# Kernel tuning notes

Measured on AMD Instinct MI355X. Metric: run time of the kernel, lower is better.

The kernel has to match this reference:

```python
import jax, jax.numpy as jnp
import numpy as np

DIM = 512
HEADS = 8
HD = DIM // HEADS
HIDDEN = 4 * DIM
EPS = 1e-5


def layernorm(x, g, b):
    mu = jnp.mean(x, axis=-1, keepdims=True)
    var = jnp.mean(jnp.square(x - mu), axis=-1, keepdims=True)
    return (x - mu) * jax.lax.rsqrt(var + EPS) * g + b


def setup_inputs() -> dict:
    key = jax.random.key(0)
    ks = jax.random.split(key, 10)
    B, P, N, C = 16, 4, 256, DIM
    s = 1.0 / np.sqrt(C)
    sh = 1.0 / np.sqrt(HIDDEN)
    return {
        "x": jax.random.normal(ks[0], (B, P, N, C), jnp.float32),
        "ln1_g": jnp.ones((C,), jnp.float32),
        "ln1_b": jnp.zeros((C,), jnp.float32),
        "w_qkv": jax.random.uniform(ks[1], (3 * C, C), jnp.float32, -s, s),
        "w_proj": jax.random.uniform(ks[2], (C, C), jnp.float32, -s, s),
        "b_proj": jax.random.uniform(ks[3], (C,), jnp.float32, -s, s),
        "ln2_g": jnp.ones((C,), jnp.float32),
        "ln2_b": jnp.zeros((C,), jnp.float32),
        "w1": jax.random.uniform(ks[4], (HIDDEN, C), jnp.float32, -s, s),
        "b1": jax.random.uniform(ks[5], (HIDDEN,), jnp.float32, -s, s),
        "w2": jax.random.uniform(ks[6], (C, HIDDEN), jnp.float32, -sh, sh),
        "b2": jax.random.uniform(ks[7], (C,), jnp.float32, -sh, sh),
    }


def reference(x, ln1_g, ln1_b, w_qkv, w_proj, b_proj, ln2_g, ln2_b, w1, b1, w2, b2):
    B, P, N, C = x.shape
    # --- attention branch (batched over B, P, heads; same math as the unrolled loops) ---
    h = layernorm(x, ln1_g, ln1_b)
    qkv = jnp.einsum('bpnc,dc->bpnd', h, w_qkv)            # [B,P,N,3C]
    qkv = qkv.reshape(B, P, N, 3, HEADS, HD)
    q, k, v = qkv[..., 0, :, :], qkv[..., 1, :, :], qkv[..., 2, :, :]  # [B,P,N,H,hd]
    scale = HD ** -0.5
    attn = jnp.einsum('bpnhd,bpmhd->bphnm', q * scale, k)  # [B,P,H,N,N]
    attn = jax.nn.softmax(attn, axis=-1)
    o = jnp.einsum('bphnm,bpmhd->bpnhd', attn, v).reshape(B, P, N, C)
    o = jnp.einsum('bpnc,dc->bpnd', o, w_proj) + b_proj
    x = x + o
    # --- MLP branch ---
    h = layernorm(x, ln2_g, ln2_b)
    h = jax.nn.gelu(jnp.einsum('bpnc,hc->bpnh', h, w1) + b1, approximate=False)
    h = jnp.einsum('bpnh,ch->bpnc', h, w2) + b2
    return x + h
```

## Files before the change

### kernel.cpp

```cpp
#include <hip/hip_runtime.h>

typedef __attribute__((ext_vector_type(8))) short short8;
typedef __attribute__((ext_vector_type(4))) float f32x4;
typedef __attribute__((ext_vector_type(4))) unsigned short u16x4;
typedef __attribute__((ext_vector_type(2))) unsigned int u32x2;

__device__ __forceinline__ float bf2f(unsigned short u) {
    return __uint_as_float(((unsigned)u) << 16);
}
__device__ __forceinline__ unsigned short f2bf(float f) {
    unsigned u = __float_as_uint(f);
    u += 0x7fffu + ((u >> 16) & 1u);
    return (unsigned short)(u >> 16);
}
__device__ __forceinline__ unsigned pack2(float lo, float hi) {
    return (unsigned)f2bf(lo) | ((unsigned)f2bf(hi) << 16);
}
__device__ __forceinline__ void load_lds16(const void* g, void* l) {
    __builtin_amdgcn_global_load_lds(
        (const __attribute__((address_space(1))) void*)g,
        (__attribute__((address_space(3))) void*)l, 16, 0, 0);
}
__device__ __forceinline__ bool is_bf16(const unsigned* dt) {
    return *dt == 0x3F803F80u;
}
__device__ __forceinline__ float gelu_fast(float t) {
    float q = t * (1.5957691f + 0.07135482f * t * t);
    float e = __expf(-q);
    return __fdividef(t, 1.0f + e);
}

__global__ __launch_bounds__(512) void cast_all(
    const void* s_wqkv, const void* s_wproj, const void* s_w1, const void* s_w2,
    const void* v0, const void* v1, const void* v2, const void* v3,
    const void* v4, const void* v5, const void* v6,
    unsigned short* d_wqkv, unsigned short* d_wproj, unsigned short* d_w1,
    unsigned short* d_w2, unsigned short* par, const unsigned* dt)
{
    bool isbf = is_bf16(dt);
    int b = blockIdx.x, tid = threadIdx.x;
    if (b < 768) {
        const void* src; unsigned short* dst; int off;
        if (b < 192)      { src = s_wqkv;  dst = d_wqkv;  off = b * 4096; }
        else if (b < 256) { src = s_wproj; dst = d_wproj; off = (b - 192) * 4096; }
        else if (b < 512) { src = s_w1;    dst = d_w1;    off = (b - 256) * 4096; }
        else              { src = s_w2;    dst = d_w2;    off = (b - 512) * 4096; }
        int i = off + tid * 8;
        if (isbf) {
            *(short8*)(dst + i) = *(const short8*)((const unsigned short*)src + i);
        } else {
            const float* s = (const float*)src + i;
            short8 o;
            #pragma unroll
            for (int j = 0; j < 8; ++j) o[j] = (short)f2bf(s[j]);
            *(short8*)(dst + i) = o;
        }
    } else {
        const void* srcs[7]  = {v0, v1, v2, v3, v4, v5, v6};
        const int   sizes[7] = {512, 512, 512, 512, 512, 2048, 512};
        const int   offs[7]  = {0, 512, 1024, 1536, 2048, 2560, 4608};
        int j = b - 768;
        const void* s = srcs[j];
        unsigned short* d = par + offs[j];
        for (int i = tid; i < sizes[j]; i += 512)
            d[i] = isbf ? ((const unsigned short*)s)[i] : f2bf(((const float*)s)[i]);
    }
}

__global__ __launch_bounds__(256) void ln_kernel(
    const void* __restrict__ xin, size_t row0,
    const unsigned* __restrict__ dt, int inmode,
    const unsigned short* __restrict__ g, const unsigned short* __restrict__ b,
    unsigned short* __restrict__ y)
{
    int w = threadIdx.x >> 6, lane = threadIdx.x & 63;
    size_t lr = (size_t)blockIdx.x * 4 + w;
    size_t gr = row0 + lr;
    bool isf32 = (inmode == 1) || (inmode == 0 && !is_bf16(dt));
    float v[8];
    if (isf32) {
        const float* xr = (const float*)xin + (gr << 9) + (lane << 3);
        #pragma unroll
        for (int j = 0; j < 8; ++j) v[j] = xr[j];
    } else {
        short8 raw = *(const short8*)((const unsigned short*)xin + (gr << 9) + (lane << 3));
        #pragma unroll
        for (int j = 0; j < 8; ++j) v[j] = bf2f((unsigned short)raw[j]);
    }
    float sum = 0.f, sq = 0.f;
    #pragma unroll
    for (int j = 0; j < 8; ++j) { sum += v[j]; sq += v[j] * v[j]; }
    #pragma unroll
    for (int off = 32; off > 0; off >>= 1) {
        sum += __shfl_xor(sum, off);
        sq  += __shfl_xor(sq, off);
    }
    float mu  = sum * (1.0f / 512.0f);
    float var = sq * (1.0f / 512.0f) - mu * mu;
    float rs  = rsqrtf(var + 1e-5f);
    short8 gr8 = *(const short8*)(g + (lane << 3));
    short8 br8 = *(const short8*)(b + (lane << 3));
    short8 outv;
    #pragma unroll
    for (int j = 0; j < 8; ++j) {
        float o = (v[j] - mu) * rs * bf2f((unsigned short)gr8[j]) + bf2f((unsigned short)br8[j]);
        outv[j] = (short)f2bf(o);
    }
    *(short8*)(y + (lr << 9) + (lane << 3)) = outv;
}

__global__ __launch_bounds__(256, 2) void gemm8(
    const unsigned short* __restrict__ A, const unsigned short* __restrict__ W,
    const unsigned short* __restrict__ bias,
    const void* __restrict__ resid, size_t rrow0,
    void* __restrict__ out, size_t orow0,
    int NBY, int N, int K, int mode, const unsigned* __restrict__ dt)
{
    constexpr int BN = 128;
    constexpr int BUFB = 32768;
    __shared__ char lds[2 * BUFB];

    int tid = threadIdx.x;
    int w = tid >> 6, lane = tid & 63;
    int l15 = lane & 15, g = lane >> 4;

    int L = blockIdx.x;
    int bx, by;
    if ((NBY & 7) == 0) {
        int nby8 = NBY >> 3;
        int xcd = L & 7, i = L >> 3;
        by = xcd * nby8 + (i % nby8);
        bx = i / nby8;
    } else {
        by = L % NBY;
        bx = L / NBY;
    }
    int m0 = by << 7, n0 = bx << 7;
    int wm = (w >> 1) << 6;
    int wn = (w & 1) << 6;

    int srow_t = tid >> 3;
    int u_t = (tid & 7) ^ (srow_t & 7);
    const unsigned short* gA[4];
    const unsigned short* gB[4];
    #pragma unroll
    for (int j = 0; j < 4; ++j) {
        gA[j] = A + (size_t)(m0 + j * 32 + srow_t) * K + u_t * 8;
        gB[j] = W + (size_t)(n0 + j * 32 + srow_t) * K + u_t * 8;
    }
    int lslot = tid * 16;
    int swz = l15 & 7;

    f32x4 acc[4][4];
    #pragma unroll
    for (int i = 0; i < 4; ++i)
        #pragma unroll
        for (int j = 0; j < 4; ++j) acc[i][j] = (f32x4){0.f, 0.f, 0.f, 0.f};

    #pragma unroll
    for (int j = 0; j < 4; ++j) {
        load_lds16(gA[j], &lds[j * 4096 + lslot]);
        load_lds16(gB[j], &lds[16384 + j * 4096 + lslot]);
    }

    int p = 0;
    for (int k = 0; k < K; k += 64) {
        __syncthreads();
        if (k + 64 < K) {
            int kn = k + 64;
            char* nb = &lds[(p ^ 1) * BUFB];
            #pragma unroll
            for (int j = 0; j < 4; ++j) {
                load_lds16(gA[j] + kn, nb + j * 4096 + lslot);
                load_lds16(gB[j] + kn, nb + 16384 + j * 4096 + lslot);
            }
        }
        const char* bAct = &lds[p * BUFB];
        const char* bW = bAct + 16384;
        #pragma unroll
        for (int s = 0; s < 2; ++s) {
            int cs = ((s * 4 + g) ^ swz) << 4;
            short8 wf[4], af[4];
            #pragma unroll
            for (int i = 0; i < 4; ++i)
                wf[i] = *(const short8*)(bW + (wn + i * 16 + l15) * 128 + cs);
            #pragma unroll
            for (int j = 0; j < 4; ++j)
                af[j] = *(const short8*)(bAct + (wm + j * 16 + l15) * 128 + cs);
            #pragma unroll
            for (int i = 0; i < 4; ++i)
                #pragma unroll
                for (int j = 0; j < 4; ++j)
                    acc[i][j] = __builtin_amdgcn_mfma_f32_16x16x32_bf16(wf[i], af[j], acc[i][j], 0, 0, 0);
        }
        p ^= 1;
    }

    if (mode == 2) {
        #pragma unroll
        for (int i = 0; i < 4; ++i) {
            u16x4 bb = *(const u16x4*)(bias + n0 + wn + i * 16 + g * 4);
            #pragma unroll
            for (int j = 0; j < 4; ++j)
                #pragma unroll
                for (int r = 0; r < 4; ++r)
                    acc[i][j][r] = gelu_fast(acc[i][j][r] + bf2f(bb[r]));
        }
    }

    char* tb = (char*)lds;
    #pragma unroll
    for (int j = 0; j < 4; ++j) {
        int mloc = wm + j * 16 + l15;
        char* rowp = tb + mloc * (BN * 2);
        int sw = mloc & (BN / 4 - 2);
        #pragma unroll
        for (int i = 0; i < 4; ++i) {
            int cq = (wn + i * 16 + g * 4) >> 2;
            u32x2 pk = {pack2(acc[i][j][0], acc[i][j][1]),
                        pack2(acc[i][j][2], acc[i][j][3])};
            *(u32x2*)(rowp + ((cq ^ sw) << 3)) = pk;
        }
    }
    __syncthreads();

    int rL = tid >> 4;
    int lc = tid & 15;
    bool inbf = is_bf16(dt);
    int colg = n0 + lc * 8;
    float bv[8];
    if (mode == 1 || mode == 3) {
        short8 bb = *(const short8*)(bias + colg);
        #pragma unroll
        for (int t = 0; t < 8; ++t) bv[t] = bf2f((unsigned short)bb[t]);
    }

    #pragma unroll
    for (int ps = 0; ps < 8; ++ps) {
        int row = ps * 16 + rL;
        int rowL = m0 + row;
        int c16 = lc ^ ((row >> 1) & 15);
        short8 vv = *(const short8*)(tb + row * (BN * 2) + (c16 << 4));

        if (mode == 0 || mode == 2) {
            *(short8*)((unsigned short*)out + (size_t)rowL * N + colg) = vv;
        } else if (mode == 1) {
            size_t rbase = (rrow0 + rowL) * (size_t)N + colg;
            float o8[8];
            if (inbf) {
                short8 rr = *(const short8*)((const unsigned short*)resid + rbase);
                #pragma unroll
                for (int t = 0; t < 8; ++t)
                    o8[t] = bf2f((unsigned short)rr[t]) + bf2f((unsigned short)vv[t]) + bv[t];
            } else {
                f32x4 r0 = *(const f32x4*)((const float*)resid + rbase);
                f32x4 r1 = *(const f32x4*)((const float*)resid + rbase + 4);
                #pragma unroll
                for (int t = 0; t < 4; ++t) {
                    o8[t]     = r0[t] + bf2f((unsigned short)vv[t]) + bv[t];
                    o8[t + 4] = r1[t] + bf2f((unsigned short)vv[t + 4]) + bv[t + 4];
                }
            }
            short8 ov;
            #pragma unroll
            for (int t = 0; t < 8; ++t) ov[t] = (short)f2bf(o8[t]);
            *(short8*)((unsigned short*)out + (size_t)rowL * N + colg) = ov;
        } else {
            size_t rbase = (size_t)rowL * N + colg;
            short8 rr = *(const short8*)((const unsigned short*)resid + rbase);
            float o8[8];
            #pragma unroll
            for (int t = 0; t < 8; ++t)
                o8[t] = bf2f((unsigned short)rr[t]) + bf2f((unsigned short)vv[t]) + bv[t];
            size_t obase = (orow0 + rowL) * (size_t)N + colg;
            if (inbf) {
                short8 ov;
                #pragma unroll
                for (int t = 0; t < 8; ++t) ov[t] = (short)f2bf(o8[t]);
                *(short8*)((unsigned short*)out + obase) = ov;
            } else {
                float* ob = (float*)out + obase;
                *(f32x4*)ob       = (f32x4){o8[0], o8[1], o8[2], o8[3]};
                *(f32x4*)(ob + 4) = (f32x4){o8[4], o8[5], o8[6], o8[7]};
            }
        }
    }
}

__global__ __launch_bounds__(256) void attn_mfma(
    const unsigned short* __restrict__ qkv, unsigned short* __restrict__ o)
{
    __shared__ unsigned short Vt[64 * 256];
    __shared__ unsigned short Ps[4][16 * 256];
    int bp = blockIdx.x >> 3, h = blockIdx.x & 7;
    const unsigned short* base = qkv + (size_t)bp * 256 * 1536;
    int qo = h << 6, ko = 512 + (h << 6), vo = 1024 + (h << 6);
    int tid = threadIdx.x, w = tid >> 6, lane = tid & 63;
    int l15 = lane & 15, g = lane >> 4;

    {
        int d = tid & 63;
        for (int s = tid >> 6; s < 256; s += 4) {
            unsigned short v = base[(size_t)s * 1536 + vo + d];
            *(unsigned short*)((char*)Vt + d * 512 + (((s >> 3) ^ (d & 7)) << 4) + ((s & 7) << 1)) = v;
        }
    }
    __syncthreads();

    unsigned short* P = Ps[w];

    for (int pass = 0; pass < 4; ++pass) {
        int q0 = pass * 64 + w * 16;
        short8 qa[2];
        #pragma unroll
        for (int t = 0; t < 2; ++t)
            qa[t] = *(const short8*)(base + (size_t)(q0 + l15) * 1536 + qo + t * 32 + g * 8);
        f32x4 S[16];
        #pragma unroll
        for (int ns = 0; ns < 16; ++ns) {
            f32x4 a = {0.f, 0.f, 0.f, 0.f};
            #pragma unroll
            for (int t = 0; t < 2; ++t) {
                short8 kb = *(const short8*)(base + (size_t)(ns * 16 + l15) * 1536 + ko + t * 32 + g * 8);
                a = __builtin_amdgcn_mfma_f32_16x16x32_bf16(qa[t], kb, a, 0, 0, 0);
            }
            S[ns] = a;
        }
        float mx[4], sums[4], inv[4];
        #pragma unroll
        for (int r = 0; r < 4; ++r) {
            float m = -1e30f;
            #pragma unroll
            for (int ns = 0; ns < 16; ++ns) m = fmaxf(m, S[ns][r]);
            m *= 0.125f;
            #pragma unroll
            for (int off = 1; off < 16; off <<= 1) m = fmaxf(m, __shfl_xor(m, off));
            mx[r] = m;
            sums[r] = 0.f;
        }
        #pragma unroll
        for (int ns = 0; ns < 16; ++ns)
            #pragma unroll
            for (int r = 0; r < 4; ++r) {
                float p = __expf(S[ns][r] * 0.125f - mx[r]);
                sums[r] += p;
                S[ns][r] = p;
            }
        #pragma unroll
        for (int r = 0; r < 4; ++r) {
            float s2 = sums[r];
            #pragma unroll
            for (int off = 1; off < 16; off <<= 1) s2 += __shfl_xor(s2, off);
            inv[r] = 1.0f / s2;
        }
        #pragma unroll
        for (int ns = 0; ns < 16; ++ns)
            #pragma unroll
            for (int r = 0; r < 4; ++r) {
                int mq = g * 4 + r;
                int s = ns * 16 + l15;
                *(unsigned short*)((char*)P + mq * 512 + (((s >> 3) ^ (mq & 7)) << 4) + ((s & 7) << 1))
                    = f2bf(S[ns][r] * inv[r]);
            }
        f32x4 O[4];
        #pragma unroll
        for (int ds = 0; ds < 4; ++ds) O[ds] = (f32x4){0.f, 0.f, 0.f, 0.f};
        #pragma unroll
        for (int ks = 0; ks < 8; ++ks) {
            int c = (ks * 4 + g) ^ (l15 & 7);
            short8 pa = *(const short8*)((const char*)P + l15 * 512 + (c << 4));
            #pragma unroll
            for (int ds = 0; ds < 4; ++ds) {
                short8 vb = *(const short8*)((const char*)Vt + (ds * 16 + l15) * 512 + (c << 4));
                O[ds] = __builtin_amdgcn_mfma_f32_16x16x32_bf16(pa, vb, O[ds], 0, 0, 0);
            }
        }
        #pragma unroll
        for (int ds = 0; ds < 4; ++ds)
            #pragma unroll
            for (int r = 0; r < 4; ++r) {
                int mq = q0 + g * 4 + r;
                int d = ds * 16 + l15;
                o[((size_t)(bp * 256 + mq) << 9) + (h << 6) + d] = f2bf(O[ds][r]);
            }
    }
}

extern "C" void kernel_launch(void* const* d_in, const int* in_sizes, int n_in,
                              void* d_out, int out_size, void* d_ws, size_t ws_size,
                              hipStream_t stream)
{
    const void* x      = d_in[0];
    const void* ln1_g  = d_in[1];
    const void* ln1_b  = d_in[2];
    const void* w_qkv  = d_in[3];
    const void* w_proj = d_in[4];
    const void* b_proj = d_in[5];
    const void* ln2_g  = d_in[6];
    const void* ln2_b  = d_in[7];
    const void* w1     = d_in[8];
    const void* b1     = d_in[9];
    const void* w2     = d_in[10];
    const void* b2     = d_in[11];
    const unsigned* dt = (const unsigned*)ln1_g;

    const int M = 16384;
    char* ws = (char*)d_ws;
    unsigned short* wqkv_b  = (unsigned short*)(ws);
    unsigned short* wproj_b = (unsigned short*)(ws + 1572864);
    unsigned short* w1_b    = (unsigned short*)(ws + 2097152);
    unsigned short* w2_b    = (unsigned short*)(ws + 4194304);
    unsigned short* par     = (unsigned short*)(ws + 6291456);
    const size_t CAST_END = 6308096;

    unsigned short* p_g1    = par + 0;
    unsigned short* p_b1ln  = par + 512;
    unsigned short* p_bproj = par + 1024;
    unsigned short* p_g2    = par + 1536;
    unsigned short* p_b2ln  = par + 2048;
    unsigned short* p_b1    = par + 2560;
    unsigned short* p_b2    = par + 4608;

    int NC = 64;
    const int cand[7] = {1, 2, 4, 8, 16, 32, 64};
    for (int i = 0; i < 7; ++i) {
        size_t need = CAST_END + (size_t)(M / cand[i]) * 10240;
        if (need <= ws_size) { NC = cand[i]; break; }
    }
    const int R = M / NC;

    char* cb = ws + CAST_END;
    unsigned short* h   = (unsigned short*)(cb);
    unsigned short* qkv = (unsigned short*)(cb + (size_t)R * 1024);
    unsigned short* o   = (unsigned short*)(cb + (size_t)R * 4096);
    unsigned short* x2  = (unsigned short*)(cb + (size_t)R * 5120);
    unsigned short* hid = (unsigned short*)(cb + (size_t)R * 6144);
    unsigned short* h2  = h;

    cast_all<<<775, 512, 0, stream>>>(w_qkv, w_proj, w1, w2,
                                      ln1_g, ln1_b, b_proj, ln2_g, ln2_b, b1, b2,
                                      wqkv_b, wproj_b, w1_b, w2_b, par, dt);

    for (int c = 0; c < NC; ++c) {
        const size_t r0 = (size_t)c * R;
        const int NBY = R / 128;

        ln_kernel<<<R / 4, 256, 0, stream>>>(x, r0, dt, 0, p_g1, p_b1ln, h);
        gemm8<<<(1536 / 128) * NBY, 256, 0, stream>>>(
            h, wqkv_b, nullptr, nullptr, 0, qkv, 0, NBY, 1536, 512, 0, dt);
        attn_mfma<<<(R / 256) * 8, 256, 0, stream>>>(qkv, o);
        gemm8<<<(512 / 128) * NBY, 256, 0, stream>>>(
            o, wproj_b, p_bproj, x, r0, x2, 0, NBY, 512, 512, 1, dt);
        ln_kernel<<<R / 4, 256, 0, stream>>>(x2, 0, dt, 2, p_g2, p_b2ln, h2);
        gemm8<<<(2048 / 128) * NBY, 256, 0, stream>>>(
            h2, w1_b, p_b1, nullptr, 0, hid, 0, NBY, 2048, 512, 2, dt);
        gemm8<<<(512 / 128) * NBY, 256, 0, stream>>>(
            hid, w2_b, p_b2, x2, 0, d_out, r0, NBY, 512, 2048, 3, dt);
    }
}
```

Before: 320.7 us.

## Use 256x128 GEMM tiles with 512 threads and triple-buffered LDS pipeline

Doubles the GEMM M tile to 256 rows and runs 8 waves per block. The K loop moves from a double-buffered to a three-stage LDS pipeline, with prefetch two steps ahead and global loads split around the MFMA phases. It also raises wave priority around the MFMA clusters and uses explicit waitcnt/barrier scheduling. The aim is more reuse of the weight tile and better overlap of loads with compute, at the cost of 144KB of LDS per block, lower occupancy and half as many blocks.

```diff
diff --git a/kernel.cpp b/kernel.cpp
--- a/kernel.cpp
+++ b/kernel.cpp
@@ -109,7 +109,7 @@
     *(short8*)(y + (lr << 9) + (lane << 3)) = outv;
 }
 
-__global__ __launch_bounds__(256, 2) void gemm8(
+__global__ __launch_bounds__(512, 2) void gemm8(
     const unsigned short* __restrict__ A, const unsigned short* __restrict__ W,
     const unsigned short* __restrict__ bias,
     const void* __restrict__ resid, size_t rrow0,
@@ -117,8 +117,8 @@
     int NBY, int N, int K, int mode, const unsigned* __restrict__ dt)
 {
     constexpr int BN = 128;
-    constexpr int BUFB = 32768;
-    __shared__ char lds[2 * BUFB];
+    constexpr int BUFB = 49152;
+    __shared__ char lds[3 * BUFB];
 
     int tid = threadIdx.x;
     int w = tid >> 6, lane = tid & 63;
@@ -135,19 +135,20 @@
         by = L % NBY;
         bx = L / NBY;
     }
-    int m0 = by << 7, n0 = bx << 7;
+    int m0 = by << 8, n0 = bx << 7;
     int wm = (w >> 1) << 6;
     int wn = (w & 1) << 6;
 
-    int srow_t = tid >> 3;
-    int u_t = (tid & 7) ^ (srow_t & 7);
+    int srow = tid >> 3;
+    int u = (tid & 7) ^ (srow & 7);
     const unsigned short* gA[4];
-    const unsigned short* gB[4];
-    #pragma unroll
-    for (int j = 0; j < 4; ++j) {
-        gA[j] = A + (size_t)(m0 + j * 32 + srow_t) * K + u_t * 8;
-        gB[j] = W + (size_t)(n0 + j * 32 + srow_t) * K + u_t * 8;
-    }
+    const unsigned short* gB[2];
+    #pragma unroll
+    for (int j = 0; j < 4; ++j)
+        gA[j] = A + (size_t)(m0 + j * 64 + srow) * K + u * 8;
+    #pragma unroll
+    for (int j = 0; j < 2; ++j)
+        gB[j] = W + (size_t)(n0 + j * 64 + srow) * K + u * 8;
     int lslot = tid * 16;
     int swz = l15 & 7;
 
@@ -157,29 +158,39 @@
         #pragma unroll
         for (int j = 0; j < 4; ++j) acc[i][j] = (f32x4){0.f, 0.f, 0.f, 0.f};
 
-    #pragma unroll
-    for (int j = 0; j < 4; ++j) {
-        load_lds16(gA[j], &lds[j * 4096 + lslot]);
-        load_lds16(gB[j], &lds[16384 + j * 4096 + lslot]);
-    }
-
-    int p = 0;
-    for (int k = 0; k < K; k += 64) {
-        __syncthreads();
-        if (k + 64 < K) {
-            int kn = k + 64;
-            char* nb = &lds[(p ^ 1) * BUFB];
-            #pragma unroll
-            for (int j = 0; j < 4; ++j) {
-                load_lds16(gA[j] + kn, nb + j * 4096 + lslot);
-                load_lds16(gB[j] + kn, nb + 16384 + j * 4096 + lslot);
-            }
-        }
-        const char* bAct = &lds[p * BUFB];
-        const char* bW = bAct + 16384;
-        #pragma unroll
-        for (int s = 0; s < 2; ++s) {
-            int cs = ((s * 4 + g) ^ swz) << 4;
+    {
+        char* b0 = lds;
+        #pragma unroll
+        for (int j = 0; j < 4; ++j) load_lds16(gA[j], b0 + j * 8192 + lslot);
+        #pragma unroll
+        for (int j = 0; j < 2; ++j) load_lds16(gB[j], b0 + 32768 + j * 8192 + lslot);
+        char* b1 = lds + BUFB;
+        #pragma unroll
+        for (int j = 0; j < 4; ++j) load_lds16(gA[j] + 64, b1 + j * 8192 + lslot);
+        #pragma unroll
+        for (int j = 0; j < 2; ++j) load_lds16(gB[j] + 64, b1 + 32768 + j * 8192 + lslot);
+    }
+    asm volatile("s_waitcnt vmcnt(6)" ::: "memory");
+    __builtin_amdgcn_s_barrier();
+    __builtin_amdgcn_sched_barrier(0);
+
+    int nk = K >> 6;
+    int bk = 0;
+    for (int k = 0; k < nk; ++k) {
+        const char* bAct = &lds[bk * BUFB];
+        const char* bW = bAct + 32768;
+        int bn2 = bk + 2; if (bn2 >= 3) bn2 -= 3;
+        char* nb = &lds[bn2 * BUFB];
+        bool hn = (k + 2 < nk);
+        int kn = (k + 2) << 6;
+
+        if (hn) {
+            load_lds16(gA[0] + kn, nb + lslot);
+            load_lds16(gA[1] + kn, nb + 8192 + lslot);
+            load_lds16(gA[2] + kn, nb + 16384 + lslot);
+        }
+        {
+            int cs = (g ^ swz) << 4;
             short8 wf[4], af[4];
             #pragma unroll
             for (int i = 0; i < 4; ++i)
@@ -187,13 +198,43 @@
             #pragma unroll
             for (int j = 0; j < 4; ++j)
                 af[j] = *(const short8*)(bAct + (wm + j * 16 + l15) * 128 + cs);
+            __builtin_amdgcn_s_setprio(1);
             #pragma unroll
             for (int i = 0; i < 4; ++i)
                 #pragma unroll
                 for (int j = 0; j < 4; ++j)
                     acc[i][j] = __builtin_amdgcn_mfma_f32_16x16x32_bf16(wf[i], af[j], acc[i][j], 0, 0, 0);
-        }
-        p ^= 1;
+            __builtin_amdgcn_s_setprio(0);
+        }
+        if (hn) {
+            load_lds16(gA[3] + kn, nb + 24576 + lslot);
+            load_lds16(gB[0] + kn, nb + 32768 + lslot);
+            load_lds16(gB[1] + kn, nb + 40960 + lslot);
+        }
+        {
+            int cs = ((4 + g) ^ swz) << 4;
+            short8 wf[4], af[4];
+            #pragma unroll
+            for (int i = 0; i < 4; ++i)
+                wf[i] = *(const short8*)(bW + (wn + i * 16 + l15) * 128 + cs);
+            #pragma unroll
+            for (int j = 0; j < 4; ++j)
+                af[j] = *(const short8*)(bAct + (wm + j * 16 + l15) * 128 + cs);
+            __builtin_amdgcn_s_setprio(1);
+            #pragma unroll
+            for (int i = 0; i < 4; ++i)
+                #pragma unroll
+                for (int j = 0; j < 4; ++j)
+                    acc[i][j] = __builtin_amdgcn_mfma_f32_16x16x32_bf16(wf[i], af[j], acc[i][j], 0, 0, 0);
+            __builtin_amdgcn_s_setprio(0);
+        }
+        __builtin_amdgcn_sched_barrier(0);
+        asm volatile("s_waitcnt lgkmcnt(0)" ::: "memory");
+        if (hn) asm volatile("s_waitcnt vmcnt(6)" ::: "memory");
+        else    asm volatile("s_waitcnt vmcnt(0)" ::: "memory");
+        __builtin_amdgcn_s_barrier();
+        __builtin_amdgcn_sched_barrier(0);
+        bk += 1; if (bk == 3) bk = 0;
     }
 
     if (mode == 2) {
@@ -237,7 +278,7 @@
 
     #pragma unroll
     for (int ps = 0; ps < 8; ++ps) {
-        int row = ps * 16 + rL;
+        int row = ps * 32 + rL;
         int rowL = m0 + row;
         int c16 = lc ^ ((row >> 1) & 15);
         short8 vv = *(const short8*)(tb + row * (BN * 2) + (c16 << 4));
@@ -443,18 +484,18 @@
 
     for (int c = 0; c < NC; ++c) {
         const size_t r0 = (size_t)c * R;
-        const int NBY = R / 128;
+        const int NBY = R / 256;
 
         ln_kernel<<<R / 4, 256, 0, stream>>>(x, r0, dt, 0, p_g1, p_b1ln, h);
-        gemm8<<<(1536 / 128) * NBY, 256, 0, stream>>>(
+        gemm8<<<(1536 / 128) * NBY, 512, 0, stream>>>(
             h, wqkv_b, nullptr, nullptr, 0, qkv, 0, NBY, 1536, 512, 0, dt);
         attn_mfma<<<(R / 256) * 8, 256, 0, stream>>>(qkv, o);
-        gemm8<<<(512 / 128) * NBY, 256, 0, stream>>>(
+        gemm8<<<(512 / 128) * NBY, 512, 0, stream>>>(
             o, wproj_b, p_bproj, x, r0, x2, 0, NBY, 512, 512, 1, dt);
         ln_kernel<<<R / 4, 256, 0, stream>>>(x2, 0, dt, 2, p_g2, p_b2ln, h2);
-        gemm8<<<(2048 / 128) * NBY, 256, 0, stream>>>(
+        gemm8<<<(2048 / 128) * NBY, 512, 0, stream>>>(
             h2, w1_b, p_b1, nullptr, 0, hid, 0, NBY, 2048, 512, 2, dt);
-        gemm8<<<(512 / 128) * NBY, 256, 0, stream>>>(
+        gemm8<<<(512 / 128) * NBY, 512, 0, stream>>>(
             hid, w2_b, p_b2, x2, 0, d_out, r0, NBY, 512, 2048, 3, dt);
     }
 }
```

New measurement: 317.3 us. No clear change (-1.0%).
